# Kernel tuning notes

Hardware: AMD Instinct MI355X
Metric: run time of the kernel (lower is better)

Reference implementation:

```python
import jax, jax.numpy as jnp
import numpy as np

KERNEL_SIZE = 16
STRIDE = 8
NEG = -1.0e9


def setup_inputs() -> dict:
    key = jax.random.key(0)
    k1, k2, k3, k4, k5 = jax.random.split(key, 5)
    B, C, L = 8, 512, 4096
    x = jax.random.normal(k1, (B, C, L), dtype=jnp.float32)
    mask = jax.random.randint(k2, (B, L), 0, 2).astype(bool)
    W = jax.random.normal(k3, (C, C), dtype=jnp.float32) * 0.02
    b = jax.random.normal(k4, (C,), dtype=jnp.float32) * 0.02
    v = jax.random.normal(k5, (C,), dtype=jnp.float32) * 0.02
    return {"x": x, "mask": mask, "W": W, "b": b, "v": v}


def reference(x, mask, W, b, v):
    # x: [B, C, L], mask: [B, L] (True = masked out)
    B, C, L = x.shape
    win, step = KERNEL_SIZE, STRIDE
    L_pool = 1 + (L - win) // step
    # per-token projection (identical across windows since proj is per-token)
    h = jnp.tanh(jnp.einsum('bcl,dc->bld', x, W) + b)      # [B, L, C]
    s = jnp.einsum('bld,d->bl', h, v)                       # [B, L]
    idx = jnp.arange(L_pool)[:, None] * step + jnp.arange(win)[None, :]
    sw = s[:, idx]
    mw = mask[:, idx]
    sw = jnp.where(mw, NEG, sw)
    w = jax.nn.softmax(sw, axis=-1)
    w = jnp.where(mw, 0.0, w)
    norm = jnp.clip(jnp.sum(w, axis=-1, keepdims=True), 1e-6, None)
    w = w / norm
    xw = x[:, :, idx]
    return jnp.einsum('bcpw,bpw->bcp', xw, w)               # [B, C, L_pool]
```

## Files before the change

### kernel.cpp

```cpp
#include <hip/hip_runtime.h>
#include <hip/hip_bf16.h>
#include <cmath>

#define Bsz 8
#define Csz 512
#define Lsz 4096
#define LPOOL 511
#define NEGV -1000000000.0f

typedef __attribute__((ext_vector_type(8))) short short8;
typedef __attribute__((ext_vector_type(4))) float float4v;

__device__ __forceinline__ float bf2f(short u) {
  unsigned int x = ((unsigned int)(unsigned short)u) << 16;
  return __builtin_bit_cast(float, x);
}

__device__ __forceinline__ void gl_lds16(const __hip_bfloat16* g, void* l) {
  __builtin_amdgcn_global_load_lds(
      (const __attribute__((address_space(1))) unsigned int*)g,
      (__attribute__((address_space(3))) unsigned int*)l, 16, 0, 0);
}

__global__ __launch_bounds__(256) void stage1(const float* __restrict__ x,
    __hip_bfloat16* __restrict__ xTs, __hip_bfloat16* __restrict__ xbf,
    const unsigned char* __restrict__ mb, int* __restrict__ flag,
    float* __restrict__ s, const float* __restrict__ W,
    __hip_bfloat16* __restrict__ Wts) {
  const int tid = threadIdx.x;
  const int bid = blockIdx.x;
  if (bid < 4096) {
    __shared__ float sX[64][65];
    const int lt = bid & 63, ct = (bid >> 6) & 7, b = bid >> 9;
    const int l0 = lt * 64;
    const float* xb = x + ((size_t)b * Csz + ct * 64) * Lsz + l0;
    #pragma unroll
    for (int it = 0; it < 4; ++it) {
      int c = it * 16 + (tid >> 4);
      int l = (tid & 15) * 4;
      *(float4*)(&sX[c][l]) = *(const float4*)(xb + (size_t)c * Lsz + l);
    }
    __syncthreads();
    #pragma unroll
    for (int it = 0; it < 2; ++it) {
      int u = it * 256 + tid;
      int cg = u >> 6, ll = u & 63;
      __hip_bfloat16 hb[8];
      #pragma unroll
      for (int j = 0; j < 8; ++j)
        hb[j] = __float2bfloat16(sX[cg * 8 + j][ll]);
      int m = b * Lsz + l0 + ll;
      int mt = m >> 7, row = m & 127;
      int cglob = ct * 64 + cg * 8;
      int ks = cglob >> 5, seg = (cglob >> 3) & 3;
      *(short8*)(xTs + (((size_t)mt * 16 + ks) * 512 + seg * 128 + row) * 8) = *(short8*)hb;
    }
    #pragma unroll
    for (int it = 0; it < 2; ++it) {
      int u = it * 256 + tid;
      int cg = u >> 3, lseg = u & 7;
      __hip_bfloat16 hb[8];
      #pragma unroll
      for (int j = 0; j < 8; ++j)
        hb[j] = __float2bfloat16(sX[cg][lseg * 8 + j]);
      *(short8*)(xbf + ((size_t)b * Csz + ct * 64 + cg) * Lsz + l0 + lseg * 8) = *(short8*)hb;
    }
  } else {
    const int pb = bid - 4096;
    if (pb == 0) {
      __shared__ int sf;
      if (tid == 0) sf = 0;
      __syncthreads();
      int f = 0;
      for (int i = tid; i < 4096; i += 256)
        if ((i & 3) && mb[i]) f = 1;
      if (f) atomicOr(&sf, 1);
      __syncthreads();
      if (tid == 0) *flag = sf;
    } else if (pb <= 32) {
      int i = (pb - 1) * 1024 + tid * 4;
      float4 z; z.x = z.y = z.z = z.w = 0.f;
      *(float4*)(s + i) = z;
    } else {
      int tg = (pb - 33) * 256 + tid;
      int d = tg >> 6, cg = tg & 63;
      float4 w0 = *(const float4*)(W + (size_t)d * 512 + cg * 8);
      float4 w1 = *(const float4*)(W + (size_t)d * 512 + cg * 8 + 4);
      __hip_bfloat16 hb[8];
      hb[0] = __float2bfloat16(w0.x); hb[1] = __float2bfloat16(w0.y);
      hb[2] = __float2bfloat16(w0.z); hb[3] = __float2bfloat16(w0.w);
      hb[4] = __float2bfloat16(w1.x); hb[5] = __float2bfloat16(w1.y);
      hb[6] = __float2bfloat16(w1.z); hb[7] = __float2bfloat16(w1.w);
      int nt = d >> 7, row = d & 127, ks = cg >> 2, seg = cg & 3;
      *(short8*)(Wts + (((size_t)nt * 16 + ks) * 512 + seg * 128 + row) * 8) = *(short8*)hb;
    }
  }
}

__global__ __launch_bounds__(256, 2) void gemm_bf16(
    const __hip_bfloat16* __restrict__ xTs, const __hip_bfloat16* __restrict__ Wts,
    const float* __restrict__ bias, const float* __restrict__ v,
    float* __restrict__ s) {
  __shared__ short8 sAv[512];
  __shared__ short8 sBv[512];
  const int tid = threadIdx.x;
  const int lane = tid & 63, wave = tid >> 6;
  const int lr = lane & 15, quad = lane >> 4;
  const int mh = wave >> 1, nh = wave & 1;
  const int mt = blockIdx.x, nt = blockIdx.y;
  const __hip_bfloat16* aT = xTs + (size_t)mt * 65536;
  const __hip_bfloat16* bT = Wts + (size_t)nt * 65536;

  float bl[4], vl[4];
  #pragma unroll
  for (int nf = 0; nf < 4; ++nf) {
    int n = nt * 128 + nh * 64 + nf * 16 + lr;
    bl[nf] = bias[n]; vl[nf] = v[n];
  }

  float4v acc[4][4];
  #pragma unroll
  for (int i = 0; i < 4; ++i)
    #pragma unroll
    for (int j = 0; j < 4; ++j) acc[i][j] = (float4v)0.f;

  for (int ks = 0; ks < 16; ++ks) {
    __syncthreads();
    const __hip_bfloat16* ga = aT + ks * 4096 + (wave * 64 + lane) * 8;
    const __hip_bfloat16* gb = bT + ks * 4096 + (wave * 64 + lane) * 8;
    gl_lds16(ga,        &sAv[wave * 64]);
    gl_lds16(ga + 2048, &sAv[256 + wave * 64]);
    gl_lds16(gb,        &sBv[wave * 64]);
    gl_lds16(gb + 2048, &sBv[256 + wave * 64]);
    __syncthreads();
    short8 af[4], bfr[4];
    #pragma unroll
    for (int mf = 0; mf < 4; ++mf)
      af[mf] = sAv[quad * 128 + mh * 64 + mf * 16 + lr];
    #pragma unroll
    for (int nf = 0; nf < 4; ++nf)
      bfr[nf] = sBv[quad * 128 + nh * 64 + nf * 16 + lr];
    #pragma unroll
    for (int mf = 0; mf < 4; ++mf)
      #pragma unroll
      for (int nf = 0; nf < 4; ++nf)
        acc[mf][nf] = __builtin_amdgcn_mfma_f32_16x16x32_bf16(af[mf], bfr[nf], acc[mf][nf], 0, 0, 0);
  }

  #pragma unroll
  for (int mf = 0; mf < 4; ++mf) {
    #pragma unroll
    for (int reg = 0; reg < 4; ++reg) {
      float p = 0.f;
      #pragma unroll
      for (int nf = 0; nf < 4; ++nf)
        p += tanhf(acc[mf][nf][reg] + bl[nf]) * vl[nf];
      p += __shfl_xor(p, 1, 16);
      p += __shfl_xor(p, 2, 16);
      p += __shfl_xor(p, 4, 16);
      p += __shfl_xor(p, 8, 16);
      if (lr == 0)
        atomicAdd(&s[mt * 128 + mh * 64 + mf * 16 + quad * 4 + reg], p);
    }
  }
}

__global__ __launch_bounds__(256) void pool2(const __hip_bfloat16* __restrict__ xbf,
    const float* __restrict__ s, const void* __restrict__ mask,
    const int* __restrict__ flag, float* __restrict__ out) {
  __shared__ float wl[8][17];
  const int t = threadIdx.x;
  const int p0 = blockIdx.x * 8, b = blockIdx.y;
  if (t < 8 && p0 + t < LPOOL) {
    const int p = p0 + t;
    const bool u8 = (*flag != 0);
    const unsigned char* m8 = (const unsigned char*)mask;
    const int* m32 = (const int*)mask;
    const int base = b * Lsz + p * 8;
    float sv[16]; int mv[16];
    float mx = -3.4e38f;
    #pragma unroll
    for (int w = 0; w < 16; ++w) {
      int mk = u8 ? (int)m8[base + w] : m32[base + w];
      float val = mk ? NEGV : s[base + w];
      sv[w] = val; mv[w] = mk;
      mx = fmaxf(mx, val);
    }
    float sum = 0.f;
    #pragma unroll
    for (int w = 0; w < 16; ++w) { sv[w] = expf(sv[w] - mx); sum += sv[w]; }
    float inv = 1.0f / sum;
    float norm = 0.f;
    #pragma unroll
    for (int w = 0; w < 16; ++w) { sv[w] = mv[w] ? 0.f : sv[w] * inv; norm += sv[w]; }
    norm = fmaxf(norm, 1e-6f);
    float rn = 1.0f / norm;
    #pragma unroll
    for (int w = 0; w < 16; ++w) wl[t][w] = sv[w] * rn;
  }
  __syncthreads();
  const int ci = t >> 3, pi = t & 7;
  const int p = p0 + pi;
  if (p >= LPOOL) return;
  float wr[16];
  #pragma unroll
  for (int w = 0; w < 16; ++w) wr[w] = wl[pi][w];
  #pragma unroll 4
  for (int it = 0; it < 16; ++it) {
    int c = it * 32 + ci;
    const __hip_bfloat16* xp = xbf + ((size_t)b * Csz + c) * Lsz + 8 * p;
    short8 lo = *(const short8*)xp;
    short8 hi = *(const short8*)(xp + 8);
    float acc = 0.f;
    #pragma unroll
    for (int j = 0; j < 8; ++j)
      acc += bf2f(lo[j]) * wr[j] + bf2f(hi[j]) * wr[8 + j];
    out[((size_t)b * Csz + c) * LPOOL + p] = acc;
  }
}

__global__ void detect_mask(const unsigned char* __restrict__ mb, int* __restrict__ flag) {
  __shared__ int sf;
  int t = threadIdx.x;
  if (t == 0) sf = 0;
  __syncthreads();
  int f = 0;
  for (int i = t; i < 4096; i += 256)
    if ((i & 3) && mb[i]) f = 1;
  if (f) atomicOr(&sf, 1);
  __syncthreads();
  if (t == 0) *flag = sf;
}

__global__ __launch_bounds__(256) void gemm_s_f32(const float* __restrict__ x,
    const float* __restrict__ W, const float* __restrict__ bias,
    const float* __restrict__ v, float* __restrict__ s_out) {
  __shared__ float sA[32][64];
  __shared__ float sB[32][68];
  __shared__ float s_acc[64];
  const int tid = threadIdx.x;
  const int b = blockIdx.y;
  const int l0 = blockIdx.x * 64;
  if (tid < 64) s_acc[tid] = 0.0f;
  const int tx = tid & 15;
  const int ty = tid >> 4;
  const float* xb = x + ((size_t)b * Csz) * Lsz + l0;
  for (int d0 = 0; d0 < Csz; d0 += 64) {
    float acc[4][4] = {{0.f}};
    for (int c0 = 0; c0 < Csz; c0 += 32) {
      __syncthreads();
      #pragma unroll
      for (int it = 0; it < 8; ++it) {
        int idx = tid + it * 256;
        int kc = idx >> 6, ml = idx & 63;
        sA[kc][ml] = xb[(size_t)(c0 + kc) * Lsz + ml];
      }
      #pragma unroll
      for (int it = 0; it < 8; ++it) {
        int idx = tid + it * 256;
        int kc = idx & 31, dj = idx >> 5;
        sB[kc][dj] = W[(size_t)(d0 + dj) * Csz + c0 + kc];
      }
      __syncthreads();
      #pragma unroll
      for (int kc = 0; kc < 32; ++kc) {
        float4 a  = *(const float4*)(&sA[kc][tx << 2]);
        float4 w4 = *(const float4*)(&sB[kc][ty << 2]);
        acc[0][0] += a.x * w4.x; acc[0][1] += a.x * w4.y; acc[0][2] += a.x * w4.z; acc[0][3] += a.x * w4.w;
        acc[1][0] += a.y * w4.x; acc[1][1] += a.y * w4.y; acc[1][2] += a.y * w4.z; acc[1][3] += a.y * w4.w;
        acc[2][0] += a.z * w4.x; acc[2][1] += a.z * w4.y; acc[2][2] += a.z * w4.z; acc[2][3] += a.z * w4.w;
        acc[3][0] += a.w * w4.x; acc[3][1] += a.w * w4.y; acc[3][2] += a.w * w4.z; acc[3][3] += a.w * w4.w;
      }
    }
    float part[4] = {0.f, 0.f, 0.f, 0.f};
    #pragma unroll
    for (int j = 0; j < 4; ++j) {
      int d = d0 + (ty << 2) + j;
      float bj = bias[d], vj = v[d];
      #pragma unroll
      for (int i = 0; i < 4; ++i)
        part[i] += tanhf(acc[i][j] + bj) * vj;
    }
    #pragma unroll
    for (int i = 0; i < 4; ++i)
      atomicAdd(&s_acc[(tx << 2) + i], part[i]);
  }
  __syncthreads();
  if (tid < 64) s_out[(size_t)b * Lsz + l0 + tid] = s_acc[tid];
}

__global__ void win_weights(const float* __restrict__ s, const void* __restrict__ mask,
                            const int* __restrict__ flag, float* __restrict__ wgt) {
  int t = blockIdx.x * blockDim.x + threadIdx.x;
  if (t >= Bsz * LPOOL) return;
  int b = t / LPOOL, p = t - b * LPOOL;
  const bool u8 = (*flag != 0);
  const unsigned char* m8 = (const unsigned char*)mask;
  const int* m32 = (const int*)mask;
  float sv[16]; int mv[16];
  float mx = -3.4e38f;
  int base = b * Lsz + p * 8;
  #pragma unroll
  for (int w = 0; w < 16; ++w) {
    int mk = u8 ? (int)m8[base + w] : m32[base + w];
    float val = mk ? NEGV : s[base + w];
    sv[w] = val; mv[w] = mk;
    mx = fmaxf(mx, val);
  }
  float sum = 0.f;
  #pragma unroll
  for (int w = 0; w < 16; ++w) { sv[w] = expf(sv[w] - mx); sum += sv[w]; }
  float inv = 1.0f / sum;
  float norm = 0.f;
  #pragma unroll
  for (int w = 0; w < 16; ++w) { sv[w] = mv[w] ? 0.f : sv[w] * inv; norm += sv[w]; }
  norm = fmaxf(norm, 1e-6f);
  float rn = 1.0f / norm;
  #pragma unroll
  for (int w = 0; w < 16; ++w) wgt[t * 16 + w] = sv[w] * rn;
}

__global__ __launch_bounds__(256) void pool_out(const float* __restrict__ x,
    const float* __restrict__ wgt, float* __restrict__ out) {
  __shared__ float xrow[Lsz];
  int bc = blockIdx.x;
  int c = bc & (Csz - 1);
  int b = bc >> 9;
  const float* xr = x + ((size_t)b * Csz + c) * Lsz;
  int tid = threadIdx.x;
  #pragma unroll
  for (int it = 0; it < 4; ++it) {
    int idx = (tid + it * 256) << 2;
    *(float4*)(&xrow[idx]) = *(const float4*)(&xr[idx]);
  }
  __syncthreads();
  const float* wb = wgt + (size_t)b * LPOOL * 16;
  float* ob = out + ((size_t)b * Csz + c) * LPOOL;
  for (int p = tid; p < LPOOL; p += 256) {
    const float4* wp = (const float4*)(wb + p * 16);
    const float4* xp = (const float4*)(&xrow[p * 8]);
    float acc = 0.f;
    #pragma unroll
    for (int q = 0; q < 4; ++q) {
      float4 wv = wp[q], xv = xp[q];
      acc += xv.x * wv.x + xv.y * wv.y + xv.z * wv.z + xv.w * wv.w;
    }
    ob[p] = acc;
  }
}

extern "C" void kernel_launch(void* const* d_in, const int* in_sizes, int n_in,
                              void* d_out, int out_size, void* d_ws, size_t ws_size,
                              hipStream_t stream) {
  const float* x    = (const float*)d_in[0];
  const void*  mask = d_in[1];
  const float* W    = (const float*)d_in[2];
  const float* bias = (const float*)d_in[3];
  const float* v    = (const float*)d_in[4];
  float* out = (float*)d_out;

  char* wsb = (char*)d_ws;
  int*   flag = (int*)wsb;
  float* s    = (float*)(wsb + 256);
  float* wgt  = (float*)(wsb + 131328);
  __hip_bfloat16* Wts = (__hip_bfloat16*)(wsb + 393216);
  __hip_bfloat16* xTs = (__hip_bfloat16*)(wsb + 917504);
  __hip_bfloat16* xbf = (__hip_bfloat16*)(wsb + 917504 + 33554432);
  const size_t NEED = 917504 + 33554432 + 33554432;

  if (ws_size >= NEED) {
    stage1<<<4096 + 161, 256, 0, stream>>>(x, xTs, xbf,
        (const unsigned char*)mask, flag, s, W, Wts);
    gemm_bf16<<<dim3(256, 4), 256, 0, stream>>>(xTs, Wts, bias, v, s);
    pool2<<<dim3(64, Bsz), 256, 0, stream>>>(xbf, s, mask, flag, out);
  } else {
    detect_mask<<<1, 256, 0, stream>>>((const unsigned char*)mask, flag);
    gemm_s_f32<<<dim3(Lsz / 64, Bsz), 256, 0, stream>>>(x, W, bias, v, s);
    win_weights<<<(Bsz * LPOOL + 255) / 256, 256, 0, stream>>>(s, mask, flag, wgt);
    pool_out<<<Bsz * Csz, 256, 0, stream>>>(x, wgt, out);
  }
}
```

Before: 158.8 us.

## Fuse x transpose/bf16 conversion into GEMM and loop all N tiles per block

```diff
diff --git a/kernel.cpp b/kernel.cpp
--- a/kernel.cpp
+++ b/kernel.cpp
@@ -16,153 +16,192 @@
   return __builtin_bit_cast(float, x);
 }
 
+__device__ __forceinline__ float ftanh(float x) {
+  float e = __expf(2.0f * x);
+  return 1.0f - 2.0f * __builtin_amdgcn_rcpf(e + 1.0f);
+}
+
 __device__ __forceinline__ void gl_lds16(const __hip_bfloat16* g, void* l) {
   __builtin_amdgcn_global_load_lds(
       (const __attribute__((address_space(1))) unsigned int*)g,
       (__attribute__((address_space(3))) unsigned int*)l, 16, 0, 0);
 }
 
-__global__ __launch_bounds__(256) void stage1(const float* __restrict__ x,
-    __hip_bfloat16* __restrict__ xTs, __hip_bfloat16* __restrict__ xbf,
-    const unsigned char* __restrict__ mb, int* __restrict__ flag,
-    float* __restrict__ s, const float* __restrict__ W,
+__global__ __launch_bounds__(256) void prep(const unsigned char* __restrict__ mb,
+    int* __restrict__ flag, const float* __restrict__ W,
     __hip_bfloat16* __restrict__ Wts) {
   const int tid = threadIdx.x;
-  const int bid = blockIdx.x;
-  if (bid < 4096) {
-    __shared__ float sX[64][65];
-    const int lt = bid & 63, ct = (bid >> 6) & 7, b = bid >> 9;
-    const int l0 = lt * 64;
-    const float* xb = x + ((size_t)b * Csz + ct * 64) * Lsz + l0;
-    #pragma unroll
-    for (int it = 0; it < 4; ++it) {
-      int c = it * 16 + (tid >> 4);
-      int l = (tid & 15) * 4;
-      *(float4*)(&sX[c][l]) = *(const float4*)(xb + (size_t)c * Lsz + l);
-    }
+  const int pb = blockIdx.x;
+  if (pb == 0) {
+    __shared__ int sf;
+    if (tid == 0) sf = 0;
     __syncthreads();
-    #pragma unroll
-    for (int it = 0; it < 2; ++it) {
-      int u = it * 256 + tid;
-      int cg = u >> 6, ll = u & 63;
-      __hip_bfloat16 hb[8];
-      #pragma unroll
-      for (int j = 0; j < 8; ++j)
-        hb[j] = __float2bfloat16(sX[cg * 8 + j][ll]);
-      int m = b * Lsz + l0 + ll;
-      int mt = m >> 7, row = m & 127;
-      int cglob = ct * 64 + cg * 8;
-      int ks = cglob >> 5, seg = (cglob >> 3) & 3;
-      *(short8*)(xTs + (((size_t)mt * 16 + ks) * 512 + seg * 128 + row) * 8) = *(short8*)hb;
-    }
-    #pragma unroll
-    for (int it = 0; it < 2; ++it) {
-      int u = it * 256 + tid;
-      int cg = u >> 3, lseg = u & 7;
-      __hip_bfloat16 hb[8];
-      #pragma unroll
-      for (int j = 0; j < 8; ++j)
-        hb[j] = __float2bfloat16(sX[cg][lseg * 8 + j]);
-      *(short8*)(xbf + ((size_t)b * Csz + ct * 64 + cg) * Lsz + l0 + lseg * 8) = *(short8*)hb;
-    }
+    int f = 0;
+    for (int i = tid; i < 4096; i += 256)
+      if ((i & 3) && mb[i]) f = 1;
+    if (f) atomicOr(&sf, 1);
+    __syncthreads();
+    if (tid == 0) *flag = sf;
   } else {
-    const int pb = bid - 4096;
-    if (pb == 0) {
-      __shared__ int sf;
-      if (tid == 0) sf = 0;
-      __syncthreads();
-      int f = 0;
-      for (int i = tid; i < 4096; i += 256)
-        if ((i & 3) && mb[i]) f = 1;
-      if (f) atomicOr(&sf, 1);
-      __syncthreads();
-      if (tid == 0) *flag = sf;
-    } else if (pb <= 32) {
-      int i = (pb - 1) * 1024 + tid * 4;
-      float4 z; z.x = z.y = z.z = z.w = 0.f;
-      *(float4*)(s + i) = z;
-    } else {
-      int tg = (pb - 33) * 256 + tid;
-      int d = tg >> 6, cg = tg & 63;
-      float4 w0 = *(const float4*)(W + (size_t)d * 512 + cg * 8);
-      float4 w1 = *(const float4*)(W + (size_t)d * 512 + cg * 8 + 4);
-      __hip_bfloat16 hb[8];
-      hb[0] = __float2bfloat16(w0.x); hb[1] = __float2bfloat16(w0.y);
-      hb[2] = __float2bfloat16(w0.z); hb[3] = __float2bfloat16(w0.w);
-      hb[4] = __float2bfloat16(w1.x); hb[5] = __float2bfloat16(w1.y);
-      hb[6] = __float2bfloat16(w1.z); hb[7] = __float2bfloat16(w1.w);
-      int nt = d >> 7, row = d & 127, ks = cg >> 2, seg = cg & 3;
-      *(short8*)(Wts + (((size_t)nt * 16 + ks) * 512 + seg * 128 + row) * 8) = *(short8*)hb;
-    }
-  }
-}
-
-__global__ __launch_bounds__(256, 2) void gemm_bf16(
-    const __hip_bfloat16* __restrict__ xTs, const __hip_bfloat16* __restrict__ Wts,
+    int tg = (pb - 1) * 256 + tid;
+    int d = tg >> 6, cg = tg & 63;
+    float4 w0 = *(const float4*)(W + (size_t)d * 512 + cg * 8);
+    float4 w1 = *(const float4*)(W + (size_t)d * 512 + cg * 8 + 4);
+    __hip_bfloat16 hb[8];
+    hb[0] = __float2bfloat16(w0.x); hb[1] = __float2bfloat16(w0.y);
+    hb[2] = __float2bfloat16(w0.z); hb[3] = __float2bfloat16(w0.w);
+    hb[4] = __float2bfloat16(w1.x); hb[5] = __float2bfloat16(w1.y);
+    hb[6] = __float2bfloat16(w1.z); hb[7] = __float2bfloat16(w1.w);
+    int nt = d >> 7, row = d & 127, ks = cg >> 2, seg = cg & 3;
+    *(short8*)(Wts + (((size_t)nt * 16 + ks) * 512 + seg * 128 + row) * 8) = *(short8*)hb;
+  }
+}
+
+__global__ __launch_bounds__(256, 1) void gemm_fused(
+    const float* __restrict__ x, const __hip_bfloat16* __restrict__ Wts,
     const float* __restrict__ bias, const float* __restrict__ v,
-    float* __restrict__ s) {
-  __shared__ short8 sAv[512];
-  __shared__ short8 sBv[512];
+    float* __restrict__ s, __hip_bfloat16* __restrict__ xbf) {
+  __shared__ short8 sA[8192];
+  __shared__ short8 sB[2][512];
+  __shared__ float  sX[4][16][33];
+
   const int tid = threadIdx.x;
   const int lane = tid & 63, wave = tid >> 6;
+  const int mt = blockIdx.x;
+  const int b = mt >> 5;
+  const int l0 = (mt & 31) << 7;
+
+  {
+    const int r = lane >> 2;
+    const int q = lane & 3;
+    const size_t rowbase = (((size_t)(b * Csz + r)) << 12) + (size_t)l0 + wave * 32 + q * 8;
+    const float* xg = x + rowbase;
+    const int ll = lane & 31, kseg = lane >> 5;
+
+    float4 a0 = *(const float4*)(xg);
+    float4 a1 = *(const float4*)(xg + 4);
+    float4 b0 = *(const float4*)(xg + (1u << 16));
+    float4 b1 = *(const float4*)(xg + (1u << 16) + 4);
+    float4 c0 = a0, c1 = a1;
+
+    for (int cc = 0; cc < 32; ++cc) {
+      if (cc < 30) {
+        const float* xn = xg + ((size_t)(cc + 2) << 16);
+        c0 = *(const float4*)(xn);
+        c1 = *(const float4*)(xn + 4);
+      }
+      __hip_bfloat16 hb[8];
+      hb[0] = __float2bfloat16(a0.x); hb[1] = __float2bfloat16(a0.y);
+      hb[2] = __float2bfloat16(a0.z); hb[3] = __float2bfloat16(a0.w);
+      hb[4] = __float2bfloat16(a1.x); hb[5] = __float2bfloat16(a1.y);
+      hb[6] = __float2bfloat16(a1.z); hb[7] = __float2bfloat16(a1.w);
+      *(short8*)(xbf + rowbase + ((size_t)cc << 16)) = *(short8*)hb;
+      *(float4*)(&sX[wave][r][q * 8])     = a0;
+      *(float4*)(&sX[wave][r][q * 8 + 4]) = a1;
+      asm volatile("s_waitcnt lgkmcnt(0)" ::: "memory");
+      __builtin_amdgcn_sched_barrier(0);
+      float tv[8];
+      #pragma unroll
+      for (int j = 0; j < 8; ++j) tv[j] = sX[wave][kseg * 8 + j][ll];
+      __hip_bfloat16 ab[8];
+      #pragma unroll
+      for (int j = 0; j < 8; ++j) ab[j] = __float2bfloat16(tv[j]);
+      const int k0 = cc * 16 + kseg * 8;
+      const int ks = k0 >> 5, seg = (k0 >> 3) & 3;
+      sA[(ks * 4 + seg) * 128 + wave * 32 + ll] = *(short8*)ab;
+      asm volatile("s_waitcnt lgkmcnt(0)" ::: "memory");
+      __builtin_amdgcn_sched_barrier(0);
+      a0 = b0; a1 = b1; b0 = c0; b1 = c1;
+    }
+  }
+
   const int lr = lane & 15, quad = lane >> 4;
-  const int mh = wave >> 1, nh = wave & 1;
-  const int mt = blockIdx.x, nt = blockIdx.y;
-  const __hip_bfloat16* aT = xTs + (size_t)mt * 65536;
-  const __hip_bfloat16* bT = Wts + (size_t)nt * 65536;
-
-  float bl[4], vl[4];
-  #pragma unroll
-  for (int nf = 0; nf < 4; ++nf) {
-    int n = nt * 128 + nh * 64 + nf * 16 + lr;
-    bl[nf] = bias[n]; vl[nf] = v[n];
-  }
-
-  float4v acc[4][4];
-  #pragma unroll
-  for (int i = 0; i < 4; ++i)
-    #pragma unroll
-    for (int j = 0; j < 4; ++j) acc[i][j] = (float4v)0.f;
-
-  for (int ks = 0; ks < 16; ++ks) {
-    __syncthreads();
-    const __hip_bfloat16* ga = aT + ks * 4096 + (wave * 64 + lane) * 8;
-    const __hip_bfloat16* gb = bT + ks * 4096 + (wave * 64 + lane) * 8;
-    gl_lds16(ga,        &sAv[wave * 64]);
-    gl_lds16(ga + 2048, &sAv[256 + wave * 64]);
-    gl_lds16(gb,        &sBv[wave * 64]);
-    gl_lds16(gb + 2048, &sBv[256 + wave * 64]);
-    __syncthreads();
-    short8 af[4], bfr[4];
-    #pragma unroll
-    for (int mf = 0; mf < 4; ++mf)
-      af[mf] = sAv[quad * 128 + mh * 64 + mf * 16 + lr];
-    #pragma unroll
-    for (int nf = 0; nf < 4; ++nf)
-      bfr[nf] = sBv[quad * 128 + nh * 64 + nf * 16 + lr];
-    #pragma unroll
-    for (int mf = 0; mf < 4; ++mf)
-      #pragma unroll
-      for (int nf = 0; nf < 4; ++nf)
-        acc[mf][nf] = __builtin_amdgcn_mfma_f32_16x16x32_bf16(af[mf], bfr[nf], acc[mf][nf], 0, 0, 0);
-  }
-
-  #pragma unroll
-  for (int mf = 0; mf < 4; ++mf) {
+  float bl[4][8], vl[4][8];
+  #pragma unroll
+  for (int nt = 0; nt < 4; ++nt)
+    #pragma unroll
+    for (int nf = 0; nf < 8; ++nf) {
+      int n = nt * 128 + nf * 16 + lr;
+      bl[nt][nf] = bias[n];
+      vl[nt][nf] = v[n];
+    }
+
+  {
+    const __hip_bfloat16* gb = Wts + (size_t)(wave * 64 + lane) * 8;
+    gl_lds16(gb,        &sB[0][wave * 64]);
+    gl_lds16(gb + 2048, &sB[0][256 + wave * 64]);
+  }
+  __syncthreads();
+
+  float4v acc[2][8];
+  float sp[2][4];
+  #pragma unroll
+  for (int mf = 0; mf < 2; ++mf) {
+    #pragma unroll
+    for (int nf = 0; nf < 8; ++nf) acc[mf][nf] = (float4v)0.f;
+    #pragma unroll
+    for (int reg = 0; reg < 4; ++reg) sp[mf][reg] = 0.f;
+  }
+
+  #pragma unroll
+  for (int nt = 0; nt < 4; ++nt) {
+    #pragma unroll 2
+    for (int ks = 0; ks < 16; ++ks) {
+      const int idx = nt * 16 + ks;
+      const int cur = idx & 1;
+      if (idx < 63) {
+        const __hip_bfloat16* gb =
+            Wts + ((size_t)(idx + 1) << 12) + (size_t)(wave * 64 + lane) * 8;
+        gl_lds16(gb,        &sB[cur ^ 1][wave * 64]);
+        gl_lds16(gb + 2048, &sB[cur ^ 1][256 + wave * 64]);
+        asm volatile("s_waitcnt vmcnt(2)" ::: "memory");
+      } else {
+        asm volatile("s_waitcnt vmcnt(0)" ::: "memory");
+      }
+      __builtin_amdgcn_sched_barrier(0);
+      __builtin_amdgcn_s_barrier();
+      short8 af[2], bfr[8];
+      #pragma unroll
+      for (int mf = 0; mf < 2; ++mf)
+        af[mf] = sA[(ks * 4 + quad) * 128 + wave * 32 + mf * 16 + lr];
+      #pragma unroll
+      for (int nf = 0; nf < 8; ++nf)
+        bfr[nf] = sB[cur][quad * 128 + nf * 16 + lr];
+      #pragma unroll
+      for (int mf = 0; mf < 2; ++mf)
+        #pragma unroll
+        for (int nf = 0; nf < 8; ++nf)
+          acc[mf][nf] = __builtin_amdgcn_mfma_f32_16x16x32_bf16(
+              af[mf], bfr[nf], acc[mf][nf], 0, 0, 0);
+      __builtin_amdgcn_s_barrier();
+    }
+    #pragma unroll
+    for (int mf = 0; mf < 2; ++mf) {
+      #pragma unroll
+      for (int reg = 0; reg < 4; ++reg) {
+        float pp = 0.f;
+        #pragma unroll
+        for (int nf = 0; nf < 8; ++nf)
+          pp += ftanh(acc[mf][nf][reg] + bl[nt][nf]) * vl[nt][nf];
+        sp[mf][reg] += pp;
+      }
+      #pragma unroll
+      for (int nf = 0; nf < 8; ++nf) acc[mf][nf] = (float4v)0.f;
+    }
+  }
+
+  #pragma unroll
+  for (int mf = 0; mf < 2; ++mf)
     #pragma unroll
     for (int reg = 0; reg < 4; ++reg) {
-      float p = 0.f;
-      #pragma unroll
-      for (int nf = 0; nf < 4; ++nf)
-        p += tanhf(acc[mf][nf][reg] + bl[nf]) * vl[nf];
-      p += __shfl_xor(p, 1, 16);
-      p += __shfl_xor(p, 2, 16);
-      p += __shfl_xor(p, 4, 16);
-      p += __shfl_xor(p, 8, 16);
+      float pv = sp[mf][reg];
+      pv += __shfl_xor(pv, 1, 16);
+      pv += __shfl_xor(pv, 2, 16);
+      pv += __shfl_xor(pv, 4, 16);
+      pv += __shfl_xor(pv, 8, 16);
       if (lr == 0)
-        atomicAdd(&s[mt * 128 + mh * 64 + mf * 16 + quad * 4 + reg], p);
-    }
-  }
+        s[mt * 128 + wave * 32 + mf * 16 + quad * 4 + reg] = pv;
+    }
 }
 
 __global__ __launch_bounds__(256) void pool2(const __hip_bfloat16* __restrict__ xbf,
@@ -364,14 +403,12 @@
   float* s    = (float*)(wsb + 256);
   float* wgt  = (float*)(wsb + 131328);
   __hip_bfloat16* Wts = (__hip_bfloat16*)(wsb + 393216);
-  __hip_bfloat16* xTs = (__hip_bfloat16*)(wsb + 917504);
-  __hip_bfloat16* xbf = (__hip_bfloat16*)(wsb + 917504 + 33554432);
-  const size_t NEED = 917504 + 33554432 + 33554432;
+  __hip_bfloat16* xbf = (__hip_bfloat16*)(wsb + 917504);
+  const size_t NEED = 917504 + 33554432;
 
   if (ws_size >= NEED) {
-    stage1<<<4096 + 161, 256, 0, stream>>>(x, xTs, xbf,
-        (const unsigned char*)mask, flag, s, W, Wts);
-    gemm_bf16<<<dim3(256, 4), 256, 0, stream>>>(xTs, Wts, bias, v, s);
+    prep<<<129, 256, 0, stream>>>((const unsigned char*)mask, flag, W, Wts);
+    gemm_fused<<<256, 256, 0, stream>>>(x, Wts, bias, v, s, xbf);
     pool2<<<dim3(64, Bsz), 256, 0, stream>>>(xbf, s, mask, flag, out);
   } else {
     detect_mask<<<1, 256, 0, stream>>>((const unsigned char*)mask, flag);
```

After: 169.9 us. 1.07x slower.
